# Kernel tuning notes

Measured on AMD Instinct MI355X. Metric: run time of the kernel, lower is better.

## Reference

```python
import jax, jax.numpy as jnp
import numpy as np

DIM = 768
H = 6        # pinned by router mask construction (3 logits -> 6 head gates)
HD = DIM // H  # 128
TAU = 5.0

def setup_inputs() -> dict:
    key = jax.random.key(0)
    ks = jax.random.split(key, 10)
    w = 0.02
    return {
        "x": jax.random.normal(ks[0], (4, 2048, DIM), jnp.float32),
        "latency": jax.random.uniform(ks[1], (1,), jnp.float32),
        "qkv_w": jax.random.normal(ks[2], (3 * DIM, DIM), jnp.float32) * w,
        "qkv_b": jax.random.normal(ks[3], (3 * DIM,), jnp.float32) * w,
        "proj_w": jax.random.normal(ks[4], (DIM, DIM), jnp.float32) * w,
        "proj_b": jax.random.normal(ks[5], (DIM,), jnp.float32) * w,
        "router_w": jax.random.normal(ks[6], (3, 1), jnp.float32),
        "router_b": jax.random.normal(ks[7], (3,), jnp.float32),
        # gumbel noise g = -log(Exp(1)), matching -empty.exponential_().log()
        "g1": -jnp.log(jax.random.exponential(ks[8], (3,), jnp.float32)),
        "g2": -jnp.log(jax.random.exponential(ks[9], (3,), jnp.float32)),
    }

def reference(x, latency, qkv_w, qkv_b, proj_w, proj_b, router_w, router_b, g1, g2):
    # router: Linear(1, 3) on scalar latency -> 3 logits
    logits = router_w @ latency + router_b                      # [3]
    # gumbel-sigmoid, tau=5, hard=True with straight-through estimator
    y_soft = jax.nn.sigmoid((logits + g1 - g2) / TAU)           # [3]
    y_hard = (y_soft > 0.5).astype(y_soft.dtype)
    mask3 = y_hard - jax.lax.stop_gradient(y_soft) + y_soft     # [3]
    # first logit gates 4 heads, remaining two gate one head each -> 6 heads
    mask6 = jnp.concatenate([mask3[:1], mask3[:1], mask3[:1], mask3])  # [6]
    maskC = jnp.repeat(mask6, HD)                               # [DIM]

    B, N, C = x.shape
    qkv = jnp.einsum('bnc,oc->bno', x, qkv_w) + qkv_b           # [B,N,3*DIM]
    qkv = qkv.reshape(B, N, 3, H, HD)
    q, k, v = qkv[:, :, 0], qkv[:, :, 1], qkv[:, :, 2]          # [B,N,H,HD]

    scale = HD ** -0.5
    attn = jax.nn.softmax(jnp.einsum('bqhd,bkhd->bhqk', q * scale, k), axis=-1)
    out = jnp.einsum('bhqk,bkhd->bqhd', attn, v).reshape(B, N, C)

    out = out * maskC                                            # gate heads/channels
    return jnp.einsum('bnc,oc->bno', out, proj_w) + proj_b
```

## Files before the change

### kernel.cpp

```cpp
#include <hip/hip_runtime.h>
#include <cstdint>

#define DIM_ 768
#define H_ 6
#define HD_ 128
#define NB_ 4
#define SEQ_ 2048
#define TOK_ (NB_*SEQ_)
#define OUT3_ (3*DIM_)
#define L2E 1.4426950408889634f

typedef __bf16 bf16;
typedef __bf16 bf16x4 __attribute__((ext_vector_type(4)));
typedef __bf16 bf16x8 __attribute__((ext_vector_type(8)));
typedef float f32x4 __attribute__((ext_vector_type(4)));
typedef float f32x16 __attribute__((ext_vector_type(16)));
typedef unsigned int u32;
typedef u32 u32x4 __attribute__((ext_vector_type(4)));

__device__ __forceinline__ void gload16(const void* g, void* lds) {
  __builtin_amdgcn_global_load_lds((const __attribute__((address_space(1))) void*)g,
                                   (__attribute__((address_space(3))) void*)lds,
                                   16, 0, 0);
}

__global__ void convert_kernel(const float* __restrict__ in, bf16* __restrict__ out, int n) {
  int i = (blockIdx.x * 256 + threadIdx.x) * 4;
  if (i >= n) return;
  float4 v = *reinterpret_cast<const float4*>(in + i);
  bf16x4 o = { (bf16)v.x, (bf16)v.y, (bf16)v.z, (bf16)v.w };
  *reinterpret_cast<bf16x4*>(out + i) = o;
}

__global__ void mask_kernel(const float* __restrict__ latency,
                            const float* __restrict__ rw,
                            const float* __restrict__ rb,
                            const float* __restrict__ g1,
                            const float* __restrict__ g2,
                            float* __restrict__ mask6) {
  int i = threadIdx.x;
  if (i < 6) {
    int j = (i < 4) ? 0 : (i - 3);
    float logit = rw[j] * latency[0] + rb[j];
    float z = (logit + g1[j] - g2[j]) / 5.0f;
    float ys = 1.0f / (1.0f + expf(-z));
    float yh = ys > 0.5f ? 1.0f : 0.0f;
    mask6[i] = (yh - ys) + ys;
  }
}


__global__ __launch_bounds__(256)
void qkv_gemm(const bf16* __restrict__ A, const bf16* __restrict__ W,
              const float* __restrict__ bias,
              bf16* __restrict__ q, bf16* __restrict__ k, bf16* __restrict__ vt) {
  __shared__ bf16 As[128 * 32];
  __shared__ bf16 Bs[128 * 32];
  __shared__ bf16 FragS[8192];
  const int tid = threadIdx.x;
  const int l = tid & 63, w = tid >> 6;
  const int lr = l & 15, lg = l >> 4;
  const int wm = w >> 1, wn = w & 1;
  const int tm = blockIdx.y * 128;
  const int on = blockIdx.x * 128;

  f32x4 acc[4][4];
#pragma unroll
  for (int i = 0; i < 4; ++i)
#pragma unroll
    for (int j = 0; j < 4; ++j) acc[i][j] = f32x4{0.f, 0.f, 0.f, 0.f};

  for (int k0 = 0; k0 < DIM_; k0 += 32) {
    __syncthreads();
#pragma unroll
    for (int u = 0; u < 2; ++u) {
      int row = w * 32 + u * 16 + (l >> 2);
      int cb = l & 3;
      gload16(A + (size_t)(tm + row) * DIM_ + k0 + cb * 8, As + (w * 32 + u * 16) * 32);
      gload16(W + (size_t)(on + row) * DIM_ + k0 + cb * 8, Bs + (w * 32 + u * 16) * 32);
    }
    __syncthreads();
    bf16x8 af[4], bfr[4];
#pragma unroll
    for (int i = 0; i < 4; ++i)
      af[i] = *reinterpret_cast<const bf16x8*>(As + (wm * 64 + i * 16 + lr) * 32 + lg * 8);
#pragma unroll
    for (int j = 0; j < 4; ++j)
      bfr[j] = *reinterpret_cast<const bf16x8*>(Bs + (wn * 64 + j * 16 + lr) * 32 + lg * 8);
#pragma unroll
    for (int i = 0; i < 4; ++i)
#pragma unroll
      for (int j = 0; j < 4; ++j)
        acc[i][j] = __builtin_amdgcn_mfma_f32_16x16x32_bf16(af[i], bfr[j], acc[i][j], 0, 0, 0);
  }

  if (on < 2 * DIM_) {
    const int s = on / DIM_;
    const float scale = 0.08838834764831845f * L2E;
    const int n0 = tm & 2047;
    const int bb = tm >> 11;
    const int hh = (on - s * DIM_) >> 7;
    const int bhh = bb * H_ + hh;
    bf16* dstbase = (s == 0) ? q : k;
    for (int pass = 0; pass < 2; ++pass) {
      __syncthreads();
      if (wm == pass) {
#pragma unroll
        for (int i = 0; i < 4; ++i) {
#pragma unroll
          for (int j = 0; j < 4; ++j) {
            int dd = wn * 64 + j * 16 + lr;
            int kc = dd >> 4, hi8 = (dd >> 3) & 1, e = dd & 7;
            float bia = bias[on + dd];
#pragma unroll
            for (int r = 0; r < 4; ++r) {
              int nl = i * 16 + lg * 4 + r;
              float val = acc[i][j][r] + bia;
              if (s == 0) val *= scale;
              FragS[(((nl >> 5) * 8 + kc) << 9) + ((hi8 * 32 + (nl & 31)) << 3) + e] = (bf16)val;
            }
          }
        }
      }
      __syncthreads();
      size_t base = ((size_t)bhh * 64 + (n0 >> 5) + pass * 2) * 4096;
#pragma unroll
      for (int r8 = 0; r8 < 4; ++r8) {
        bf16x8 v8 = *reinterpret_cast<const bf16x8*>(FragS + r8 * 2048 + tid * 8);
        *reinterpret_cast<bf16x8*>(dstbase + base + r8 * 2048 + tid * 8) = v8;
      }
    }
  } else {
    const int hh = (on - 2 * DIM_) >> 7;
    const int bb = tm >> 11, n0 = tm & 2047;
    const int bhh = bb * H_ + hh;
    bf16(*Ts)[136] = reinterpret_cast<bf16(*)[136]>(As);
    for (int wc = 0; wc < 2; ++wc) {
#pragma unroll
      for (int j = 0; j < 4; ++j) {
        __syncthreads();
        if (wn == wc) {
          float bia = bias[on + wc * 64 + j * 16 + lr];
#pragma unroll
          for (int i = 0; i < 4; ++i) {
            bf16x4 pk;
#pragma unroll
            for (int r = 0; r < 4; ++r) pk[r] = (bf16)(acc[i][j][r] + bia);
            *reinterpret_cast<bf16x4*>(&Ts[lr][wm * 64 + i * 16 + lg * 4]) = pk;
          }
        }
        __syncthreads();
        int row = tid >> 4;
        int c8 = (tid & 15) * 8;
        bf16x8 v8 = *reinterpret_cast<const bf16x8*>(&Ts[row][c8]);
        int d = wc * 64 + j * 16 + row;
        int n = n0 + c8;
        size_t idx = (((((size_t)bhh * 32 + (n >> 6)) * 4 + ((n >> 4) & 3)) * 4 + (d >> 5)) << 9) +
                     ((((n >> 3) & 1) * 32 + (d & 31)) << 3);
        *reinterpret_cast<bf16x8*>(vt + idx) = v8;
      }
    }
  }
}

__global__ __launch_bounds__(256)
void proj_gemm(const bf16* __restrict__ A, const bf16* __restrict__ W,
               const float* __restrict__ bias, float* __restrict__ out) {
  __shared__ bf16 As[128 * 32];
  __shared__ bf16 Bs[128 * 32];
  const int tid = threadIdx.x;
  const int l = tid & 63, w = tid >> 6;
  const int lr = l & 15, lg = l >> 4;
  const int wm = w >> 1, wn = w & 1;
  const int tm = blockIdx.y * 128;
  const int on = blockIdx.x * 128;

  f32x4 acc[4][4];
#pragma unroll
  for (int i = 0; i < 4; ++i)
#pragma unroll
    for (int j = 0; j < 4; ++j) acc[i][j] = f32x4{0.f, 0.f, 0.f, 0.f};

  for (int k0 = 0; k0 < DIM_; k0 += 32) {
    __syncthreads();
#pragma unroll
    for (int u = 0; u < 2; ++u) {
      int row = w * 32 + u * 16 + (l >> 2);
      int cb = l & 3;
      gload16(A + (size_t)(tm + row) * DIM_ + k0 + cb * 8, As + (w * 32 + u * 16) * 32);
      gload16(W + (size_t)(on + row) * DIM_ + k0 + cb * 8, Bs + (w * 32 + u * 16) * 32);
    }
    __syncthreads();
    bf16x8 af[4], bfr[4];
#pragma unroll
    for (int i = 0; i < 4; ++i)
      af[i] = *reinterpret_cast<const bf16x8*>(As + (wm * 64 + i * 16 + lr) * 32 + lg * 8);
#pragma unroll
    for (int j = 0; j < 4; ++j)
      bfr[j] = *reinterpret_cast<const bf16x8*>(Bs + (wn * 64 + j * 16 + lr) * 32 + lg * 8);
#pragma unroll
    for (int i = 0; i < 4; ++i)
#pragma unroll
      for (int j = 0; j < 4; ++j)
        acc[i][j] = __builtin_amdgcn_mfma_f32_16x16x32_bf16(af[i], bfr[j], acc[i][j], 0, 0, 0);
  }

#pragma unroll
  for (int i = 0; i < 4; ++i) {
#pragma unroll
    for (int j = 0; j < 4; ++j) {
      int o = on + wn * 64 + j * 16 + lr;
      float bia = bias[o];
#pragma unroll
      for (int r = 0; r < 4; ++r) {
        int t = tm + wm * 64 + i * 16 + lg * 4 + r;
        out[(size_t)t * DIM_ + o] = acc[i][j][r] + bia;
      }
    }
  }
}

__global__ __launch_bounds__(128)
void attn_kernel(const bf16* __restrict__ qf_g, const bf16* __restrict__ kf_g,
                 const bf16* __restrict__ vf_g, const float* __restrict__ mask6,
                 bf16* __restrict__ ab) {
  __shared__ bf16 KS[2][4096];
  __shared__ bf16 VS[2][4096];

  const int tid = threadIdx.x;
  const int l = tid & 63;
  const int wq = tid >> 6;
  const int kl = l & 31;
  const int hi = l >> 5;
  const int bid = blockIdx.x;
  const int bh = bid % 24;
  const int qt2 = bid / 24;
  const int h = bh % H_;
  const int b = bh / H_;
  const int q0 = qt2 * 64 + wq * 32;
  const int loff = l * 8;

  const bf16* qq = qf_g + (((size_t)bh * 64 + qt2 * 2 + wq) * 8) * 512;
  const bf16* kq = kf_g + (size_t)bh * 262144;
  const bf16* vq = vf_g + (size_t)bh * 262144;

  bf16x8 qf[8];
#pragma unroll
  for (int kc = 0; kc < 8; ++kc)
    qf[kc] = *reinterpret_cast<const bf16x8*>(qq + kc * 512 + loff);

  f32x16 oacc[4];
#pragma unroll
  for (int df = 0; df < 4; ++df)
#pragma unroll
    for (int r = 0; r < 16; ++r) oacc[df][r] = 0.f;
  float m_lane = -3.0e38f;
  float lsum = 0.f;

  auto STAGE = [&](int jj, int buf) {
    const bf16* kb = kq + (size_t)jj * 4096;
    const bf16* vb = vq + (size_t)jj * 4096;
#pragma unroll
    for (int u = 0; u < 4; ++u) {
      int c = wq * 4 + u;
      gload16(kb + c * 512 + loff, &KS[buf][c * 512]);
      gload16(vb + c * 512 + loff, &VS[buf][c * 512]);
    }
  };

  STAGE(0, 0);
  __syncthreads();

  for (int jj = 0; jj < 64; ++jj) {
    int cur = jj & 1;
    STAGE((jj + 1) & 63, cur ^ 1);

    const bf16* Kc = &KS[cur][0];
    const bf16* Vc = &VS[cur][0];

    f32x16 sacc;
#pragma unroll
    for (int r = 0; r < 16; ++r) sacc[r] = 0.f;
    __builtin_amdgcn_s_setprio(1);
#pragma unroll
    for (int kc = 0; kc < 8; ++kc) {
      bf16x8 kfr = *reinterpret_cast<const bf16x8*>(Kc + kc * 512 + loff);
      sacc = __builtin_amdgcn_mfma_f32_32x32x16_bf16(kfr, qf[kc], sacc, 0, 0, 0);
    }
    __builtin_amdgcn_s_setprio(0);

    float t = sacc[0];
#pragma unroll
    for (int r = 1; r < 16; ++r) t = fmaxf(t, sacc[r]);
    t = fmaxf(t, __shfl_xor(t, 32));
    bool need = t > m_lane + 8.0f;
    if (__ballot(need) != 0ull) {
      float nm = fmaxf(m_lane, t);
      float c = exp2f(m_lane - nm);
      m_lane = nm;
      lsum *= c;
#pragma unroll
      for (int r = 0; r < 16; ++r) {
        float cr = __shfl(c, (r & 3) + 8 * (r >> 2) + 4 * hi);
#pragma unroll
        for (int df = 0; df < 4; ++df) oacc[df][r] *= cr;
      }
    }

    u32 pp[8];
#pragma unroll
    for (int m = 0; m < 8; ++m) {
      float e0 = exp2f(sacc[2 * m] - m_lane);
      float e1 = exp2f(sacc[2 * m + 1] - m_lane);
      lsum += e0 + e1;
      union { u32 u; bf16 hh2[2]; } pk;
      pk.hh2[0] = (bf16)e0; pk.hh2[1] = (bf16)e1;
      pp[m] = pk.u;
    }

    u32x4 afv[2];
#pragma unroll
    for (int ks = 0; ks < 2; ++ks) {
#pragma unroll
      for (int i = 0; i < 2; ++i) {
        u32 a = pp[4 * ks + i];
        u32 b2 = pp[4 * ks + 2 + i];
        asm volatile("v_permlane32_swap_b32 %0, %1" : "+v"(a), "+v"(b2));
        afv[ks][i] = a;
        afv[ks][2 + i] = b2;
      }
    }

    __builtin_amdgcn_s_setprio(1);
#pragma unroll
    for (int ks = 0; ks < 2; ++ks) {
      bf16x8 pa = __builtin_bit_cast(bf16x8, afv[ks]);
#pragma unroll
      for (int df = 0; df < 4; ++df) {
        bf16x8 vfr = *reinterpret_cast<const bf16x8*>(Vc + (ks * 4 + df) * 512 + loff);
        oacc[df] = __builtin_amdgcn_mfma_f32_32x32x16_bf16(pa, vfr, oacc[df], 0, 0, 0);
      }
    }
    __builtin_amdgcn_s_setprio(0);

    __syncthreads();
  }

  float lt = lsum + __shfl_xor(lsum, 32);
  float hm = mask6[h];
  float inv_l = hm / lt;
#pragma unroll
  for (int r = 0; r < 16; ++r) {
    int qloc = (r & 3) + 8 * (r >> 2) + 4 * hi;
    float invr = __shfl(inv_l, qloc);
    int n = q0 + qloc;
#pragma unroll
    for (int df = 0; df < 4; ++df) {
      int d = df * 32 + kl;
      ab[((size_t)b * SEQ_ + n) * DIM_ + h * HD_ + d] = (bf16)(oacc[df][r] * invr);
    }
  }
}

extern "C" void kernel_launch(void* const* d_in, const int* in_sizes, int n_in,
                              void* d_out, int out_size, void* d_ws, size_t ws_size,
                              hipStream_t stream) {
  const float* x        = (const float*)d_in[0];
  const float* latency  = (const float*)d_in[1];
  const float* qkv_w    = (const float*)d_in[2];
  const float* qkv_b    = (const float*)d_in[3];
  const float* proj_w   = (const float*)d_in[4];
  const float* proj_b   = (const float*)d_in[5];
  const float* router_w = (const float*)d_in[6];
  const float* router_b = (const float*)d_in[7];
  const float* g1       = (const float*)d_in[8];
  const float* g2       = (const float*)d_in[9];
  float* out = (float*)d_out;

  const size_t N_X  = (size_t)TOK_ * DIM_;
  const size_t N_WQ = (size_t)OUT3_ * DIM_;
  const size_t N_WP = (size_t)DIM_ * DIM_;
  const size_t N_P  = (size_t)NB_ * H_ * SEQ_ * HD_;

  float* maskp = (float*)d_ws;
  bf16* xb  = (bf16*)((char*)d_ws + 256);
  bf16* wqb = xb + N_X;
  bf16* wpb = wqb + N_WQ;
  bf16* qbf = wpb + N_WP;
  bf16* kbf = qbf + N_P;
  bf16* vtb = kbf + N_P;
  bf16* abf = vtb + N_P;

  size_t need = 256 + 2 * (N_X + N_WQ + N_WP + 4 * N_P);
  if (ws_size < need) return;

  convert_kernel<<<(int)(N_X / 1024), 256, 0, stream>>>(x, xb, (int)N_X);
  convert_kernel<<<(int)(N_WQ / 1024), 256, 0, stream>>>(qkv_w, wqb, (int)N_WQ);
  convert_kernel<<<(int)(N_WP / 1024), 256, 0, stream>>>(proj_w, wpb, (int)N_WP);
  mask_kernel<<<1, 64, 0, stream>>>(latency, router_w, router_b, g1, g2, maskp);

  qkv_gemm<<<dim3(OUT3_ / 128, TOK_ / 128), 256, 0, stream>>>(xb, wqb, qkv_b, qbf, kbf, vtb);
  attn_kernel<<<dim3(24 * (SEQ_ / 64)), 128, 0, stream>>>(qbf, kbf, vtb, maskp, abf);
  proj_gemm<<<dim3(DIM_ / 128, TOK_ / 128), 256, 0, stream>>>(abf, wpb, proj_b, out);
}
```

Measured before the change: 197.2 us.

## Split KV range across two wave pairs and skip masked-out heads in attention

Attention blocks now use four waves: two halves each process half the key/value sequence for the same 64 queries, and partial outputs are merged via LDS using log-sum-exp rescaling. Heads whose gate mask is zero write zeros and exit early. Double buffering of K/V loads is replaced by load-then-sync per iteration, trading prefetch overlap for shorter per-block serial loops and more waves in flight.

```diff
diff --git a/kernel.cpp b/kernel.cpp
--- a/kernel.cpp
+++ b/kernel.cpp
@@ -220,27 +220,42 @@
   }
 }
 
-__global__ __launch_bounds__(128)
+__global__ __launch_bounds__(256)
 void attn_kernel(const bf16* __restrict__ qf_g, const bf16* __restrict__ kf_g,
                  const bf16* __restrict__ vf_g, const float* __restrict__ mask6,
                  bf16* __restrict__ ab) {
-  __shared__ bf16 KS[2][4096];
-  __shared__ bf16 VS[2][4096];
+  __shared__ char smem[33280];
 
   const int tid = threadIdx.x;
   const int l = tid & 63;
-  const int wq = tid >> 6;
-  const int kl = l & 31;
-  const int hi = l >> 5;
+  const int w = tid >> 6;
+  const int half = w >> 1, qw = w & 1;
+  const int kl = l & 31, hi = l >> 5;
   const int bid = blockIdx.x;
   const int bh = bid % 24;
   const int qt2 = bid / 24;
   const int h = bh % H_;
   const int b = bh / H_;
-  const int q0 = qt2 * 64 + wq * 32;
+  const int q0 = qt2 * 64 + qw * 32;
   const int loff = l * 8;
-
-  const bf16* qq = qf_g + (((size_t)bh * 64 + qt2 * 2 + wq) * 8) * 512;
+  const float hm = mask6[h];
+
+  if (hm == 0.0f) {
+    bf16x8 z = __builtin_bit_cast(bf16x8, u32x4{0u, 0u, 0u, 0u});
+    int row = tid >> 2, c0 = (tid & 3) * 32;
+    bf16* dst = ab + ((size_t)b * SEQ_ + qt2 * 64 + row) * DIM_ + h * HD_ + c0;
+#pragma unroll
+    for (int u = 0; u < 4; ++u)
+      *reinterpret_cast<bf16x8*>(dst + u * 8) = z;
+    return;
+  }
+
+  bf16* KSh = (bf16*)(smem + half * 8192);
+  bf16* VSh = (bf16*)(smem + 16384 + half * 8192);
+  float* MLm = (float*)(smem + 32768);
+  float* MLl = MLm + 64;
+
+  const bf16* qq = qf_g + (((size_t)bh * 64 + qt2 * 2 + qw) * 8) * 512;
   const bf16* kq = kf_g + (size_t)bh * 262144;
   const bf16* vq = vf_g + (size_t)bh * 262144;
 
@@ -257,26 +272,15 @@
   float m_lane = -3.0e38f;
   float lsum = 0.f;
 
-  auto STAGE = [&](int jj, int buf) {
-    const bf16* kb = kq + (size_t)jj * 4096;
-    const bf16* vb = vq + (size_t)jj * 4096;
+  for (int it = 0; it < 32; ++it) {
+    int jj = half * 32 + it;
 #pragma unroll
     for (int u = 0; u < 4; ++u) {
-      int c = wq * 4 + u;
-      gload16(kb + c * 512 + loff, &KS[buf][c * 512]);
-      gload16(vb + c * 512 + loff, &VS[buf][c * 512]);
-    }
-  };
-
-  STAGE(0, 0);
-  __syncthreads();
-
-  for (int jj = 0; jj < 64; ++jj) {
-    int cur = jj & 1;
-    STAGE((jj + 1) & 63, cur ^ 1);
-
-    const bf16* Kc = &KS[cur][0];
-    const bf16* Vc = &VS[cur][0];
+      int c = qw * 4 + u;
+      gload16(kq + (size_t)jj * 4096 + c * 512 + loff, KSh + c * 512);
+      gload16(vq + (size_t)jj * 4096 + c * 512 + loff, VSh + c * 512);
+    }
+    __syncthreads();
 
     f32x16 sacc;
 #pragma unroll
@@ -284,7 +288,7 @@
     __builtin_amdgcn_s_setprio(1);
 #pragma unroll
     for (int kc = 0; kc < 8; ++kc) {
-      bf16x8 kfr = *reinterpret_cast<const bf16x8*>(Kc + kc * 512 + loff);
+      bf16x8 kfr = *reinterpret_cast<const bf16x8*>(KSh + kc * 512 + loff);
       sacc = __builtin_amdgcn_mfma_f32_32x32x16_bf16(kfr, qf[kc], sacc, 0, 0, 0);
     }
     __builtin_amdgcn_s_setprio(0);
@@ -337,7 +341,7 @@
       bf16x8 pa = __builtin_bit_cast(bf16x8, afv[ks]);
 #pragma unroll
       for (int df = 0; df < 4; ++df) {
-        bf16x8 vfr = *reinterpret_cast<const bf16x8*>(Vc + (ks * 4 + df) * 512 + loff);
+        bf16x8 vfr = *reinterpret_cast<const bf16x8*>(VSh + (ks * 4 + df) * 512 + loff);
         oacc[df] = __builtin_amdgcn_mfma_f32_32x32x16_bf16(pa, vfr, oacc[df], 0, 0, 0);
       }
     }
@@ -347,17 +351,41 @@
   }
 
   float lt = lsum + __shfl_xor(lsum, 32);
-  float hm = mask6[h];
-  float inv_l = hm / lt;
+
+  float* OM = (float*)smem;
+  if (half == 1) {
+#pragma unroll
+    for (int r = 0; r < 16; ++r) {
+      int qloc = (r & 3) + 8 * (r >> 2) + 4 * hi;
+#pragma unroll
+      for (int df = 0; df < 4; ++df)
+        OM[qw * 4096 + qloc * 128 + df * 32 + kl] = oacc[df][r];
+    }
+    MLm[qw * 32 + kl] = m_lane;
+    MLl[qw * 32 + kl] = lt;
+  }
+  __syncthreads();
+  if (half == 1) return;
+
+  float m1 = MLm[qw * 32 + kl];
+  float l1 = MLl[qw * 32 + kl];
+  float M = fmaxf(m_lane, m1);
+  float a0 = exp2f(m_lane - M), a1 = exp2f(m1 - M);
+  float L = lt * a0 + l1 * a1;
+  float s0 = a0 * hm / L, s1 = a1 * hm / L;
+
 #pragma unroll
   for (int r = 0; r < 16; ++r) {
     int qloc = (r & 3) + 8 * (r >> 2) + 4 * hi;
-    float invr = __shfl(inv_l, qloc);
+    float r0 = __shfl(s0, qloc);
+    float r1 = __shfl(s1, qloc);
     int n = q0 + qloc;
 #pragma unroll
     for (int df = 0; df < 4; ++df) {
       int d = df * 32 + kl;
-      ab[((size_t)b * SEQ_ + n) * DIM_ + h * HD_ + d] = (bf16)(oacc[df][r] * invr);
+      float o1 = OM[qw * 4096 + qloc * 128 + df * 32 + kl];
+      ab[((size_t)b * SEQ_ + n) * DIM_ + h * HD_ + d] =
+          (bf16)(oacc[df][r] * r0 + o1 * r1);
     }
   }
 }
@@ -400,6 +428,6 @@
   mask_kernel<<<1, 64, 0, stream>>>(latency, router_w, router_b, g1, g2, maskp);
 
   qkv_gemm<<<dim3(OUT3_ / 128, TOK_ / 128), 256, 0, stream>>>(xb, wqb, qkv_b, qbf, kbf, vtb);
-  attn_kernel<<<dim3(24 * (SEQ_ / 64)), 128, 0, stream>>>(qbf, kbf, vtb, maskp, abf);
+  attn_kernel<<<dim3(24 * (SEQ_ / 64)), 256, 0, stream>>>(qbf, kbf, vtb, maskp, abf);
   proj_gemm<<<dim3(DIM_ / 128, TOK_ / 128), 256, 0, stream>>>(abf, wpb, proj_b, out);
 }
```

Measured after the change: 195.6 us. Within noise of the previous version (-0.8%).
